# Kernel optimization log

Measured on AMD Instinct MI355X. Metric: run time of the kernel, lower is better.

The kernel has to match this reference:

```python
import jax, jax.numpy as jnp
import numpy as np

NEG_INF = -1e38


def wkv(k, v, w, u):
    """Log-sum-exp-stabilized RWKV WKV scan.
    k, v: (B, T, C); w, u: (C,). Returns y: (B, T, C).
    """
    B, T, C = k.shape

    def step(carry, kv_t):
        num, den, mx = carry            # each (B, C)
        k_t, v_t = kv_t                 # (B, C)
        ku = k_t + u
        m = jnp.maximum(mx, ku)
        e1 = jnp.exp(mx - m)
        e2 = jnp.exp(ku - m)
        y = (e1 * num + e2 * v_t) / (e1 * den + e2)
        # state update
        mw = mx + w
        m2 = jnp.maximum(mw, k_t)
        es1 = jnp.exp(mw - m2)
        es2 = jnp.exp(k_t - m2)
        num = es1 * num + es2 * v_t
        den = es1 * den + es2
        return (num, den, m2), y

    init = (jnp.zeros((B, C), k.dtype),
            jnp.zeros((B, C), k.dtype),
            jnp.full((B, C), NEG_INF, k.dtype))
    _, y = jax.lax.scan(step, init, (jnp.swapaxes(k, 0, 1), jnp.swapaxes(v, 0, 1)))
    return jnp.swapaxes(y, 0, 1)


def setup_inputs() -> dict:
    key = jax.random.key(0)
    ks = jax.random.split(key, 8)
    B, T, C = 8, 4096, 512
    x = jax.random.normal(ks[0], (B, T, C), dtype=jnp.float32)
    # Linear weights stored as (in, out) so forward is x @ W.
    W_rkv = jax.random.normal(ks[1], (C, 6 * C), dtype=jnp.float32) / np.sqrt(C)
    W_out = jax.random.normal(ks[2], (2 * C, C), dtype=jnp.float32) / np.sqrt(2 * C)
    time_decay = jax.random.uniform(ks[3], (C,), minval=-6.0, maxval=-5.0, dtype=jnp.float32)
    time_first = jax.random.uniform(ks[4], (C,), minval=-3.0, maxval=0.0, dtype=jnp.float32)
    time_decay_rev = jax.random.uniform(ks[5], (C,), minval=-6.0, maxval=-5.0, dtype=jnp.float32)
    time_first_rev = jax.random.uniform(ks[6], (C,), minval=-3.0, maxval=0.0, dtype=jnp.float32)
    return {"x": x, "W_rkv": W_rkv, "W_out": W_out,
            "time_decay": time_decay, "time_first": time_first,
            "time_decay_rev": time_decay_rev, "time_first_rev": time_first_rev}


def reference(x, W_rkv, W_out, time_decay, time_first, time_decay_rev, time_first_rev):
    B, T, C = x.shape
    rkv = (x @ W_rkv).reshape(B, T, 2, 3, C)
    # forward direction
    r_f, k_f, v_f = rkv[:, :, 0, 0], rkv[:, :, 0, 1], rkv[:, :, 0, 2]
    w_f = -jnp.exp(time_decay)
    out_f = jax.nn.sigmoid(r_f) * wkv(k_f, v_f, w_f, time_first)
    # backward direction (run scan on time-reversed k/v, then reverse back)
    r_b, k_b, v_b = rkv[:, :, 1, 0], rkv[:, :, 1, 1], rkv[:, :, 1, 2]
    w_b = -jnp.exp(time_decay_rev)
    out_b = wkv(k_b[:, ::-1], v_b[:, ::-1], w_b, time_first_rev)[:, ::-1]
    out_b = jax.nn.sigmoid(r_b) * out_b
    out_cat = jnp.concatenate([out_f, out_b], axis=-1)  # (B, T, 2C)
    return out_cat @ W_out
```

## Files before the change

kernel.cpp:

```cpp
#include <hip/hip_runtime.h>

typedef float f4 __attribute__((ext_vector_type(4)));
typedef unsigned short us4 __attribute__((ext_vector_type(4)));
typedef __bf16 bf16x8 __attribute__((ext_vector_type(8)));
typedef float f32x4 __attribute__((ext_vector_type(4)));
typedef _Float16 h8 __attribute__((ext_vector_type(8)));

#define TT 4096
#define CCH 512
#define NCH2 256
#define CHL2 16
#define NSEG 32
#define SEGC 8

__device__ __forceinline__ unsigned short f2bf(float f) {
  unsigned u = __builtin_bit_cast(unsigned, f);
  unsigned r = (u + 0x7FFFu + ((u >> 16) & 1u)) >> 16;
  return (unsigned short)r;
}
__device__ __forceinline__ void gload_lds16(const void* g, void* l) {
  __builtin_amdgcn_global_load_lds(
      (const __attribute__((address_space(1))) unsigned int*)g,
      (__attribute__((address_space(3))) unsigned int*)l, 16, 0, 0);
}
#define VMCNT(n) asm volatile("s_waitcnt vmcnt(" #n ")" ::: "memory")

__global__ __launch_bounds__(256)
void convert_f32_bf16(const float* __restrict__ in, unsigned short* __restrict__ out, int n4) {
  int i = blockIdx.x * 256 + threadIdx.x;
  if (i >= n4) return;
  f4 f = *(const f4*)(in + (size_t)i * 4);
  us4 o = { f2bf(f[0]), f2bf(f[1]), f2bf(f[2]), f2bf(f[3]) };
  *(us4*)(out + (size_t)i * 4) = o;
}

__global__ __launch_bounds__(256)
void transpose_to_bf16(const float* __restrict__ in, unsigned short* __restrict__ out,
                       int R, int Cc) {
  __shared__ unsigned short tile[32][33];
  int c0 = blockIdx.x * 32, r0 = blockIdx.y * 32;
  int tx = threadIdx.x, ty = threadIdx.y;
  #pragma unroll
  for (int j = 0; j < 32; j += 8)
    tile[ty + j][tx] = f2bf(in[(size_t)(r0 + ty + j) * Cc + c0 + tx]);
  __syncthreads();
  #pragma unroll
  for (int j = 0; j < 32; j += 8)
    out[(size_t)(c0 + ty + j) * R + r0 + tx] = tile[tx][ty + j];
}

__global__ __launch_bounds__(256)
void transpose_to_f16(const float* __restrict__ in, _Float16* __restrict__ out,
                      int R, int Cc) {
  __shared__ _Float16 tile[32][33];
  int c0 = blockIdx.x * 32, r0 = blockIdx.y * 32;
  int tx = threadIdx.x, ty = threadIdx.y;
  #pragma unroll
  for (int j = 0; j < 32; j += 8)
    tile[ty + j][tx] = (_Float16)in[(size_t)(r0 + ty + j) * Cc + c0 + tx];
  __syncthreads();
  #pragma unroll
  for (int j = 0; j < 32; j += 8)
    out[(size_t)(c0 + ty + j) * R + r0 + tx] = tile[tx][ty + j];
}

__global__ __launch_bounds__(512, 2)
void gemm256_g1(const unsigned short* __restrict__ A,
                const unsigned short* __restrict__ BT,
                _Float16* __restrict__ kbuf, _Float16* __restrict__ vbuf,
                _Float16* __restrict__ rbuf) {
  __shared__ char lds[131072];
  const int tid = threadIdx.x;
  const int lane = tid & 63, wv = tid >> 6;
  const int wm = wv >> 2, wn = wv & 3;
  const int ln15 = lane & 15, lq = lane >> 4;

  const int nwg = gridDim.x;
  const int bid = blockIdx.x;
  const int wgid = (nwg % 8 == 0) ? (bid % 8) * (nwg / 8) + bid / 8 : bid;
  const int bn = wgid % 12, bm = wgid / 12;
  const size_t m0 = (size_t)bm * 256, n0 = (size_t)bn * 256;
  const char* Ab = (const char*)(A + m0 * 512);
  const char* Bb = (const char*)(BT + n0 * 512);

  const int srow0 = tid >> 2, srow1 = 128 + (tid >> 2);
  const int sg = tid & 3;
  const int sgs0 = (sg ^ ((srow0 >> 1) & 3)) << 4;
  const int sgs1 = (sg ^ ((srow1 >> 1) & 3)) << 4;

  auto STAGE = [&](int mat, int t, int h) {
    const char* gsrc = mat ? Bb : Ab;
    char* ldst = lds + mat * 65536 + ((t & 1) << 15) + (h << 14);
    const size_t co = (size_t)t * 128 + (size_t)h * 64;
    gload_lds16(gsrc + (size_t)srow0 * 1024 + co + sgs0, ldst + tid * 16);
    gload_lds16(gsrc + (size_t)srow1 * 1024 + co + sgs1, ldst + 8192 + tid * 16);
  };

  f32x4 acc[8][4] = {};
  STAGE(0, 0, 0); STAGE(1, 0, 0); STAGE(0, 0, 1); STAGE(1, 0, 1);

  for (int t = 0; t < 8; ++t) {
    char* Abase = lds + ((t & 1) << 15);
    char* Bbase = lds + 65536 + ((t & 1) << 15);
    VMCNT(4);
    __builtin_amdgcn_s_barrier();
    __builtin_amdgcn_sched_barrier(0);
    {
      bf16x8 bf[4], af[8];
      #pragma unroll
      for (int fn = 0; fn < 4; ++fn) {
        const int r = wn * 64 + fn * 16 + ln15;
        bf[fn] = *(const bf16x8*)(Bbase + r * 64 + ((lq ^ ((r >> 1) & 3)) << 4));
      }
      #pragma unroll
      for (int fm = 0; fm < 8; ++fm) {
        const int r = wm * 128 + fm * 16 + ln15;
        af[fm] = *(const bf16x8*)(Abase + r * 64 + ((lq ^ ((r >> 1) & 3)) << 4));
      }
      if (t < 7) { STAGE(0, t + 1, 0); STAGE(1, t + 1, 0); }
      __builtin_amdgcn_s_setprio(1);
      #pragma unroll
      for (int fm = 0; fm < 8; ++fm)
        #pragma unroll
        for (int fn = 0; fn < 4; ++fn)
          acc[fm][fn] = __builtin_amdgcn_mfma_f32_16x16x32_bf16(af[fm], bf[fn], acc[fm][fn], 0, 0, 0);
      __builtin_amdgcn_s_setprio(0);
    }
    if (t < 7) { VMCNT(4); } else { VMCNT(0); }
    __builtin_amdgcn_s_barrier();
    __builtin_amdgcn_sched_barrier(0);
    {
      bf16x8 bf[4], af[8];
      #pragma unroll
      for (int fn = 0; fn < 4; ++fn) {
        const int r = wn * 64 + fn * 16 + ln15;
        bf[fn] = *(const bf16x8*)(Bbase + 16384 + r * 64 + ((lq ^ ((r >> 1) & 3)) << 4));
      }
      #pragma unroll
      for (int fm = 0; fm < 8; ++fm) {
        const int r = wm * 128 + fm * 16 + ln15;
        af[fm] = *(const bf16x8*)(Abase + 16384 + r * 64 + ((lq ^ ((r >> 1) & 3)) << 4));
      }
      if (t < 7) { STAGE(0, t + 1, 1); STAGE(1, t + 1, 1); }
      __builtin_amdgcn_s_setprio(1);
      #pragma unroll
      for (int fm = 0; fm < 8; ++fm)
        #pragma unroll
        for (int fn = 0; fn < 4; ++fn)
          acc[fm][fn] = __builtin_amdgcn_mfma_f32_16x16x32_bf16(af[fm], bf[fn], acc[fm][fn], 0, 0, 0);
      __builtin_amdgcn_s_setprio(0);
    }
  }

  const int n0i = (int)n0;
  const int dir = (n0i >= 1536) ? 1 : 0;
  const int jj0 = n0i - dir * 1536;
  const int seg = jj0 >> 9;
  const int cbase = jj0 & 511;
  _Float16* dbuf = (seg == 0) ? rbuf : (seg == 1 ? kbuf : vbuf);
  float* stg = (float*)lds;
  const int ebnd = wv >> 2;
  const int erow = (tid >> 3) & 31;
  const int el8 = tid & 7;
  __syncthreads();
  #pragma unroll
  for (int gi = 0; gi < 4; ++gi) {
    #pragma unroll
    for (int f2 = 0; f2 < 2; ++f2) {
      const int fm = gi * 2 + f2;
      #pragma unroll
      for (int q = 0; q < 4; ++q) {
        const int rloc = f2 * 16 + lq * 4 + q;
        float* dst = stg + wm * 8192 + rloc * 256;
        const int sw = ((rloc >> 2) & 1) << 4;
        #pragma unroll
        for (int fn = 0; fn < 4; ++fn)
          dst[(wn * 64 + fn * 16 + ln15) ^ sw] = acc[fm][fn][q];
      }
    }
    __syncthreads();
    {
      const int rowg = (int)m0 + ebnd * 128 + gi * 32 + erow;
      const int b_ = rowg >> 12, tt = rowg & 4095;
      const int trow = dir ? (4095 - tt) : tt;
      _Float16* gp = dbuf + ((size_t)(b_ * 2 + dir) * TT + trow) * 512 + cbase;
      const float* sp = stg + ebnd * 8192 + erow * 256;
      const int sw = ((erow >> 2) & 1) << 4;
      #pragma unroll
      for (int u = 0; u < 4; ++u) {
        const int cf = el8 * 8 + u * 64;
        const int cs = cf ^ sw;
        f4 a = *(const f4*)(sp + cs);
        f4 b = *(const f4*)(sp + cs + 4);
        h8 hv = { (_Float16)a[0], (_Float16)a[1], (_Float16)a[2], (_Float16)a[3],
                  (_Float16)b[0], (_Float16)b[1], (_Float16)b[2], (_Float16)b[3] };
        *(h8*)(gp + cf) = hv;
      }
    }
    __syncthreads();
  }
}

__global__ __launch_bounds__(512, 2)
void gemm2_256(const _Float16* __restrict__ obuf,
               const _Float16* __restrict__ BT,
               float* __restrict__ out) {
  __shared__ char lds[131072];
  const int tid = threadIdx.x;
  const int lane = tid & 63, wv = tid >> 6;
  const int wm = wv >> 2, wn = wv & 3;
  const int ln15 = lane & 15, lq = lane >> 4;

  const int nwg = gridDim.x;
  const int bid = blockIdx.x;
  const int wgid = (nwg % 8 == 0) ? (bid % 8) * (nwg / 8) + bid / 8 : bid;
  const int bn = wgid % 2, bm = wgid / 2;
  const size_t m0 = (size_t)bm * 256, n0 = (size_t)bn * 256;
  const int bB = (int)(m0 >> 12);
  const int tbase = (int)(m0 & 4095);
  const char* Bb = (const char*)(BT + n0 * 1024);

  const int srow0 = tid >> 2, srow1 = 128 + (tid >> 2);
  const int sg = tid & 3;
  const int sgs0 = (sg ^ ((srow0 >> 1) & 3)) << 4;
  const int sgs1 = (sg ^ ((srow1 >> 1) & 3)) << 4;

  auto STAGE = [&](int mat, int t, int h) {
    char* ldst = lds + mat * 65536 + ((t & 1) << 15) + (h << 14);
    if (mat == 0) {
      const int half = t >> 3;
      const char* Ah = (const char*)(obuf + (((size_t)(bB * 2 + half)) << 12) * 512);
      const size_t co = (size_t)(t & 7) * 128 + (size_t)h * 64;
      const size_t ar0 = half ? (size_t)(4095 - (tbase + srow0)) : (size_t)(tbase + srow0);
      const size_t ar1 = half ? (size_t)(4095 - (tbase + srow1)) : (size_t)(tbase + srow1);
      gload_lds16(Ah + ar0 * 1024 + co + sgs0, ldst + tid * 16);
      gload_lds16(Ah + ar1 * 1024 + co + sgs1, ldst + 8192 + tid * 16);
    } else {
      const size_t co = (size_t)t * 128 + (size_t)h * 64;
      gload_lds16(Bb + (size_t)srow0 * 2048 + co + sgs0, ldst + tid * 16);
      gload_lds16(Bb + (size_t)srow1 * 2048 + co + sgs1, ldst + 8192 + tid * 16);
    }
  };

  f32x4 acc[8][4] = {};
  STAGE(0, 0, 0); STAGE(1, 0, 0); STAGE(0, 0, 1); STAGE(1, 0, 1);

  for (int t = 0; t < 16; ++t) {
    char* Abase = lds + ((t & 1) << 15);
    char* Bbase = lds + 65536 + ((t & 1) << 15);
    VMCNT(4);
    __builtin_amdgcn_s_barrier();
    __builtin_amdgcn_sched_barrier(0);
    {
      h8 bf[4], af[8];
      #pragma unroll
      for (int fn = 0; fn < 4; ++fn) {
        const int r = wn * 64 + fn * 16 + ln15;
        bf[fn] = *(const h8*)(Bbase + r * 64 + ((lq ^ ((r >> 1) & 3)) << 4));
      }
      #pragma unroll
      for (int fm = 0; fm < 8; ++fm) {
        const int r = wm * 128 + fm * 16 + ln15;
        af[fm] = *(const h8*)(Abase + r * 64 + ((lq ^ ((r >> 1) & 3)) << 4));
      }
      if (t < 15) { STAGE(0, t + 1, 0); STAGE(1, t + 1, 0); }
      __builtin_amdgcn_s_setprio(1);
      #pragma unroll
      for (int fm = 0; fm < 8; ++fm)
        #pragma unroll
        for (int fn = 0; fn < 4; ++fn)
          acc[fm][fn] = __builtin_amdgcn_mfma_f32_16x16x32_f16(af[fm], bf[fn], acc[fm][fn], 0, 0, 0);
      __builtin_amdgcn_s_setprio(0);
    }
    if (t < 15) { VMCNT(4); } else { VMCNT(0); }
    __builtin_amdgcn_s_barrier();
    __builtin_amdgcn_sched_barrier(0);
    {
      h8 bf[4], af[8];
      #pragma unroll
      for (int fn = 0; fn < 4; ++fn) {
        const int r = wn * 64 + fn * 16 + ln15;
        bf[fn] = *(const h8*)(Bbase + 16384 + r * 64 + ((lq ^ ((r >> 1) & 3)) << 4));
      }
      #pragma unroll
      for (int fm = 0; fm < 8; ++fm) {
        const int r = wm * 128 + fm * 16 + ln15;
        af[fm] = *(const h8*)(Abase + 16384 + r * 64 + ((lq ^ ((r >> 1) & 3)) << 4));
      }
      if (t < 15) { STAGE(0, t + 1, 1); STAGE(1, t + 1, 1); }
      __builtin_amdgcn_s_setprio(1);
      #pragma unroll
      for (int fm = 0; fm < 8; ++fm)
        #pragma unroll
        for (int fn = 0; fn < 4; ++fn)
          acc[fm][fn] = __builtin_amdgcn_mfma_f32_16x16x32_f16(af[fm], bf[fn], acc[fm][fn], 0, 0, 0);
      __builtin_amdgcn_s_setprio(0);
    }
  }

  float* stg = (float*)lds;
  const int ebnd = wv >> 2;
  const int erow = (tid >> 3) & 31;
  const int el8 = tid & 7;
  __syncthreads();
  #pragma unroll
  for (int gi = 0; gi < 4; ++gi) {
    #pragma unroll
    for (int f2 = 0; f2 < 2; ++f2) {
      const int fm = gi * 2 + f2;
      #pragma unroll
      for (int q = 0; q < 4; ++q) {
        const int rloc = f2 * 16 + lq * 4 + q;
        float* dst = stg + wm * 8192 + rloc * 256;
        const int sw = ((rloc >> 2) & 1) << 4;
        #pragma unroll
        for (int fn = 0; fn < 4; ++fn)
          dst[(wn * 64 + fn * 16 + ln15) ^ sw] = acc[fm][fn][q];
      }
    }
    __syncthreads();
    {
      const int rowg = (int)m0 + ebnd * 128 + gi * 32 + erow;
      float* gp = out + (size_t)rowg * 512 + n0;
      const float* sp = stg + ebnd * 8192 + erow * 256;
      const int sw = ((erow >> 2) & 1) << 4;
      #pragma unroll
      for (int u = 0; u < 4; ++u) {
        const int cf = el8 * 8 + u * 64;
        const int cs = cf ^ sw;
        f4 a = *(const f4*)(sp + cs);
        f4 b = *(const f4*)(sp + cs + 4);
        *(f4*)(gp + cf) = a;
        *(f4*)(gp + cf + 4) = b;
      }
    }
    __syncthreads();
  }
}

__global__ __launch_bounds__(128)
void wkv_pass1(const _Float16* __restrict__ kbuf, const _Float16* __restrict__ vbuf,
               const float* __restrict__ td, const float* __restrict__ tdr,
               float* __restrict__ cN, float* __restrict__ cD, float* __restrict__ cM) {
  const int bd = blockIdx.x;
  const int ch = blockIdx.y * 2 + threadIdx.y;
  const int dir = bd & 1;
  const int c = threadIdx.x * 8;
  const float* tdp = (dir ? tdr : td) + c;
  float w[8], num[8], den[8], m[8];
  #pragma unroll
  for (int e = 0; e < 8; ++e) { w[e] = -__expf(tdp[e]); num[e] = 0.f; den[e] = 0.f; m[e] = -1e38f; }
  const size_t base = ((size_t)bd * TT + (size_t)ch * CHL2) * CCH + c;
  const _Float16* kp = kbuf + base;
  const _Float16* vp = vbuf + base;
  h8 ka = *(const h8*)(kp), va = *(const h8*)(vp);
  h8 kb = *(const h8*)(kp + CCH), vb = *(const h8*)(vp + CCH);
  for (int t = 0; t < CHL2; ++t) {
    h8 kc = {}, vc = {};
    if (t + 2 < CHL2) {
      kc = *(const h8*)(kp + (size_t)(t + 2) * CCH);
      vc = *(const h8*)(vp + (size_t)(t + 2) * CCH);
    }
    #pragma unroll
    for (int e = 0; e < 8; ++e) {
      float ke = (float)ka[e], ve = (float)va[e];
      float mw = m[e] + w[e];
      float m2 = fmaxf(mw, ke);
      float e1 = __expf(mw - m2), e2 = __expf(ke - m2);
      num[e] = e1 * num[e] + e2 * ve;
      den[e] = e1 * den[e] + e2;
      m[e] = m2;
    }
    ka = kb; va = vb; kb = kc; vb = vc;
  }
  const size_t ci = ((size_t)bd * NCH2 + ch) * CCH + c;
  #pragma unroll
  for (int h = 0; h < 2; ++h) {
    *(f4*)(cN + ci + h * 4) = (f4){num[h*4], num[h*4+1], num[h*4+2], num[h*4+3]};
    *(f4*)(cD + ci + h * 4) = (f4){den[h*4], den[h*4+1], den[h*4+2], den[h*4+3]};
    *(f4*)(cM + ci + h * 4) = (f4){m[h*4], m[h*4+1], m[h*4+2], m[h*4+3]};
  }
}

__global__ __launch_bounds__(128)
void wkv_p2a(const float* __restrict__ td, const float* __restrict__ tdr,
             const float* __restrict__ cN, const float* __restrict__ cD,
             const float* __restrict__ cM,
             float* __restrict__ scN, float* __restrict__ scD, float* __restrict__ scM) {
  const int bd = blockIdx.x, seg = blockIdx.y;
  const int dir = bd & 1;
  const int c = threadIdx.x * 4;
  f4 tdv = *(const f4*)((dir ? tdr : td) + c);
  float dw[4], num[4], den[4], m[4];
  #pragma unroll
  for (int e = 0; e < 4; ++e) { dw[e] = -__expf(tdv[e]) * (float)CHL2; num[e] = 0.f; den[e] = 0.f; m[e] = -1e38f; }
  size_t ci = ((size_t)bd * NCH2 + (size_t)seg * SEGC) * CCH + c;
  for (int j = 0; j < SEGC; ++j, ci += CCH) {
    f4 ln = *(const f4*)(cN + ci);
    f4 ld = *(const f4*)(cD + ci);
    f4 lm = *(const f4*)(cM + ci);
    #pragma unroll
    for (int e = 0; e < 4; ++e) {
      float mp = m[e] + dw[e];
      float mm = fmaxf(mp, lm[e]);
      float e1 = __expf(mp - mm), e2 = __expf(lm[e] - mm);
      num[e] = e1 * num[e] + e2 * ln[e];
      den[e] = e1 * den[e] + e2 * ld[e];
      m[e] = mm;
    }
  }
  const size_t si = ((size_t)bd * NSEG + seg) * CCH + c;
  *(f4*)(scN + si) = (f4){num[0], num[1], num[2], num[3]};
  *(f4*)(scD + si) = (f4){den[0], den[1], den[2], den[3]};
  *(f4*)(scM + si) = (f4){m[0], m[1], m[2], m[3]};
}

__global__ __launch_bounds__(128)
void wkv_p2b(const float* __restrict__ td, const float* __restrict__ tdr,
             float* __restrict__ scN, float* __restrict__ scD, float* __restrict__ scM) {
  const int bd = blockIdx.x;
  const int dir = bd & 1;
  const int c = threadIdx.x * 4;
  f4 tdv = *(const f4*)((dir ? tdr : td) + c);
  float dws[4], num[4], den[4], m[4];
  #pragma unroll
  for (int e = 0; e < 4; ++e) { dws[e] = -__expf(tdv[e]) * (float)(CHL2 * SEGC); num[e] = 0.f; den[e] = 0.f; m[e] = -1e38f; }
  size_t si = (size_t)bd * NSEG * CCH + c;
  for (int s = 0; s < NSEG; ++s, si += CCH) {
    f4 ln = *(const f4*)(scN + si);
    f4 ld = *(const f4*)(scD + si);
    f4 lm = *(const f4*)(scM + si);
    *(f4*)(scN + si) = (f4){num[0], num[1], num[2], num[3]};
    *(f4*)(scD + si) = (f4){den[0], den[1], den[2], den[3]};
    *(f4*)(scM + si) = (f4){m[0], m[1], m[2], m[3]};
    #pragma unroll
    for (int e = 0; e < 4; ++e) {
      float mp = m[e] + dws[e];
      float mm = fmaxf(mp, lm[e]);
      float e1 = __expf(mp - mm), e2 = __expf(lm[e] - mm);
      num[e] = e1 * num[e] + e2 * ln[e];
      den[e] = e1 * den[e] + e2 * ld[e];
      m[e] = mm;
    }
  }
}

__global__ __launch_bounds__(128)
void wkv_p2c(const float* __restrict__ td, const float* __restrict__ tdr,
             const float* __restrict__ scN, const float* __restrict__ scD,
             const float* __restrict__ scM,
             float* __restrict__ cN, float* __restrict__ cD, float* __restrict__ cM) {
  const int bd = blockIdx.x, seg = blockIdx.y;
  const int dir = bd & 1;
  const int c = threadIdx.x * 4;
  f4 tdv = *(const f4*)((dir ? tdr : td) + c);
  const size_t si = ((size_t)bd * NSEG + seg) * CCH + c;
  f4 nv = *(const f4*)(scN + si);
  f4 dv = *(const f4*)(scD + si);
  f4 mv = *(const f4*)(scM + si);
  float dw[4], num[4], den[4], m[4];
  #pragma unroll
  for (int e = 0; e < 4; ++e) {
    dw[e] = -__expf(tdv[e]) * (float)CHL2;
    num[e] = nv[e]; den[e] = dv[e]; m[e] = mv[e];
  }
  size_t ci = ((size_t)bd * NCH2 + (size_t)seg * SEGC) * CCH + c;
  for (int j = 0; j < SEGC; ++j, ci += CCH) {
    f4 ln = *(const f4*)(cN + ci);
    f4 ld = *(const f4*)(cD + ci);
    f4 lm = *(const f4*)(cM + ci);
    *(f4*)(cN + ci) = (f4){num[0], num[1], num[2], num[3]};
    *(f4*)(cD + ci) = (f4){den[0], den[1], den[2], den[3]};
    *(f4*)(cM + ci) = (f4){m[0], m[1], m[2], m[3]};
    #pragma unroll
    for (int e = 0; e < 4; ++e) {
      float mp = m[e] + dw[e];
      float mm = fmaxf(mp, lm[e]);
      float e1 = __expf(mp - mm), e2 = __expf(lm[e] - mm);
      num[e] = e1 * num[e] + e2 * ln[e];
      den[e] = e1 * den[e] + e2 * ld[e];
      m[e] = mm;
    }
  }
}

__global__ __launch_bounds__(128)
void wkv_pass3(const _Float16* __restrict__ kbuf, const _Float16* __restrict__ vbuf,
               _Float16* __restrict__ rbuf,
               const float* __restrict__ td, const float* __restrict__ tf,
               const float* __restrict__ tdr, const float* __restrict__ tfr,
               const float* __restrict__ cN, const float* __restrict__ cD,
               const float* __restrict__ cM) {
  const int bd = blockIdx.x;
  const int ch = blockIdx.y * 2 + threadIdx.y;
  const int dir = bd & 1;
  const int c = threadIdx.x * 8;
  const float* tdp = (dir ? tdr : td) + c;
  const float* tup = (dir ? tfr : tf) + c;
  const size_t ci = ((size_t)bd * NCH2 + ch) * CCH + c;
  float w[8], u[8], num[8], den[8], m[8];
  #pragma unroll
  for (int e = 0; e < 8; ++e) {
    w[e] = -__expf(tdp[e]); u[e] = tup[e];
    num[e] = cN[ci + e]; den[e] = cD[ci + e]; m[e] = cM[ci + e];
  }
  const size_t base = ((size_t)bd * TT + (size_t)ch * CHL2) * CCH + c;
  const _Float16* kp = kbuf + base;
  const _Float16* vp = vbuf + base;
  _Float16* rp = rbuf + base;
  h8 ka = *(const h8*)(kp), va = *(const h8*)(vp), ra = *(const h8*)(rp);
  h8 kb = *(const h8*)(kp + CCH), vb = *(const h8*)(vp + CCH), rb = *(const h8*)(rp + CCH);
  for (int t = 0; t < CHL2; ++t) {
    h8 kc = {}, vc = {}, rc = {};
    if (t + 2 < CHL2) {
      kc = *(const h8*)(kp + (size_t)(t + 2) * CCH);
      vc = *(const h8*)(vp + (size_t)(t + 2) * CCH);
      rc = *(const h8*)(rp + (size_t)(t + 2) * CCH);
    }
    _Float16 o[8];
    #pragma unroll
    for (int e = 0; e < 8; ++e) {
      float ke = (float)ka[e], ve = (float)va[e];
      float ku = ke + u[e];
      float mm = fmaxf(m[e], ku);
      float e1 = __expf(m[e] - mm), e2 = __expf(ku - mm);
      float y = (e1 * num[e] + e2 * ve) * __builtin_amdgcn_rcpf(e1 * den[e] + e2);
      float rt = (float)ra[e];
      float sig = __builtin_amdgcn_rcpf(1.f + __expf(-rt));
      o[e] = (_Float16)(sig * y);
      float mw = m[e] + w[e];
      float m2 = fmaxf(mw, ke);
      float es1 = __expf(mw - m2), es2 = __expf(ke - m2);
      num[e] = es1 * num[e] + es2 * ve;
      den[e] = es1 * den[e] + es2;
      m[e] = m2;
    }
    h8 ov = { o[0], o[1], o[2], o[3], o[4], o[5], o[6], o[7] };
    *(h8*)(rp + (size_t)t * CCH) = ov;
    ka = kb; va = vb; ra = rb; kb = kc; vb = vc; rb = rc;
  }
}

extern "C" void kernel_launch(void* const* d_in, const int* in_sizes, int n_in,
                              void* d_out, int out_size, void* d_ws, size_t ws_size,
                              hipStream_t stream) {
  const float* x   = (const float*)d_in[0];
  const float* Wr  = (const float*)d_in[1];
  const float* Wo  = (const float*)d_in[2];
  const float* td  = (const float*)d_in[3];
  const float* tf  = (const float*)d_in[4];
  const float* tdr = (const float*)d_in[5];
  const float* tfr = (const float*)d_in[6];
  float* out = (float*)d_out;

  auto rnd = [](size_t b) { return (b + 255) & ~(size_t)255; };
  const size_t wBytes = rnd((size_t)3072 * 512 * 2) + rnd((size_t)512 * 1024 * 2);
  auto need = [&](int Bs) {
    size_t s = wBytes;
    s += 3 * rnd((size_t)Bs * 2 * TT * 512 * 2);
    s += rnd((size_t)Bs * TT * 512 * 2);
    return s;
  };
  int Bs = 8;
  while (Bs > 1 && need(Bs) > ws_size) Bs >>= 1;

  char* ws = (char*)d_ws;
  size_t off = 0;
  auto alloc = [&](size_t bytes) -> char* {
    char* p = ws + off;
    off += (bytes + 255) & ~(size_t)255;
    return p;
  };
  unsigned short* wrkvT = (unsigned short*)alloc((size_t)3072 * 512 * 2);
  _Float16*       woutT = (_Float16*)alloc((size_t)512 * 1024 * 2);
  _Float16*       kbuf  = (_Float16*)alloc((size_t)Bs * 2 * TT * 512 * 2);
  _Float16*       vbuf  = (_Float16*)alloc((size_t)Bs * 2 * TT * 512 * 2);
  _Float16*       rbuf  = (_Float16*)alloc((size_t)Bs * 2 * TT * 512 * 2);
  unsigned short* xb    = (unsigned short*)alloc((size_t)Bs * TT * 512 * 2);
  const size_t cs = (size_t)Bs * 2 * NCH2 * 512;
  const size_t ss = (size_t)Bs * 2 * NSEG * 512;
  float* cN  = (float*)xb;
  float* cD  = cN + cs;
  float* cM  = cD + cs;
  float* scN = cM + cs;
  float* scD = scN + ss;
  float* scM = scD + ss;

  transpose_to_bf16<<<dim3(3072 / 32, 512 / 32), dim3(32, 8), 0, stream>>>(Wr, wrkvT, 512, 3072);
  transpose_to_f16<<<dim3(512 / 32, 1024 / 32), dim3(32, 8), 0, stream>>>(Wo, woutT, 1024, 512);

  const int nslices = 8 / Bs;
  const int Mslice = Bs * TT;
  const int mt256 = Mslice >> 8;
  for (int s = 0; s < nslices; ++s) {
    const float* xs = x + (size_t)s * Mslice * 512;
    float* outs = out + (size_t)s * Mslice * 512;
    convert_f32_bf16<<<Mslice * 512 / 1024, 256, 0, stream>>>(xs, xb, Mslice * 512 / 4);
    gemm256_g1<<<mt256 * 12, 512, 0, stream>>>(xb, wrkvT, kbuf, vbuf, rbuf);
    wkv_pass1<<<dim3(Bs * 2, NCH2 / 2), dim3(64, 2), 0, stream>>>(kbuf, vbuf, td, tdr, cN, cD, cM);
    wkv_p2a<<<dim3(Bs * 2, NSEG), 128, 0, stream>>>(td, tdr, cN, cD, cM, scN, scD, scM);
    wkv_p2b<<<Bs * 2, 128, 0, stream>>>(td, tdr, scN, scD, scM);
    wkv_p2c<<<dim3(Bs * 2, NSEG), 128, 0, stream>>>(td, tdr, scN, scD, scM, cN, cD, cM);
    wkv_pass3<<<dim3(Bs * 2, NCH2 / 2), dim3(64, 2), 0, stream>>>(kbuf, vbuf, rbuf, td, tf, tdr, tfr,
                                                                  cN, cD, cM);
    gemm2_256<<<mt256 * 2, 512, 0, stream>>>(rbuf, woutT, outs);
  }
}
```

Before: 301.1 us.

## Fuse three-kernel chunk-state prefix scan into one per-channel kernel

Replaces the three-stage prefix (segment reduce, segment scan, segment apply) with a single kernel. Each thread handles one channel and keeps the segment carries in shared memory. This removes two kernel launches and the global-memory round trip for the segment states. In exchange, each thread does a much longer serial dependent chain, with scalar loads and far fewer blocks, which reduces parallelism.

```diff
diff --git a/kernel.cpp b/kernel.cpp
--- a/kernel.cpp
+++ b/kernel.cpp
@@ -383,103 +383,46 @@
 }
 
 __global__ __launch_bounds__(128)
-void wkv_p2a(const float* __restrict__ td, const float* __restrict__ tdr,
-             const float* __restrict__ cN, const float* __restrict__ cD,
-             const float* __restrict__ cM,
-             float* __restrict__ scN, float* __restrict__ scD, float* __restrict__ scM) {
-  const int bd = blockIdx.x, seg = blockIdx.y;
+void wkv_pass2f(const float* __restrict__ td, const float* __restrict__ tdr,
+                float* __restrict__ cN, float* __restrict__ cD, float* __restrict__ cM) {
+  __shared__ float sN[NSEG][128], sD[NSEG][128], sM[NSEG][128];
+  const int bd = blockIdx.x, cg = blockIdx.y;
   const int dir = bd & 1;
-  const int c = threadIdx.x * 4;
-  f4 tdv = *(const f4*)((dir ? tdr : td) + c);
-  float dw[4], num[4], den[4], m[4];
-  #pragma unroll
-  for (int e = 0; e < 4; ++e) { dw[e] = -__expf(tdv[e]) * (float)CHL2; num[e] = 0.f; den[e] = 0.f; m[e] = -1e38f; }
-  size_t ci = ((size_t)bd * NCH2 + (size_t)seg * SEGC) * CCH + c;
-  for (int j = 0; j < SEGC; ++j, ci += CCH) {
-    f4 ln = *(const f4*)(cN + ci);
-    f4 ld = *(const f4*)(cD + ci);
-    f4 lm = *(const f4*)(cM + ci);
-    #pragma unroll
-    for (int e = 0; e < 4; ++e) {
-      float mp = m[e] + dw[e];
-      float mm = fmaxf(mp, lm[e]);
-      float e1 = __expf(mp - mm), e2 = __expf(lm[e] - mm);
-      num[e] = e1 * num[e] + e2 * ln[e];
-      den[e] = e1 * den[e] + e2 * ld[e];
-      m[e] = mm;
-    }
-  }
-  const size_t si = ((size_t)bd * NSEG + seg) * CCH + c;
-  *(f4*)(scN + si) = (f4){num[0], num[1], num[2], num[3]};
-  *(f4*)(scD + si) = (f4){den[0], den[1], den[2], den[3]};
-  *(f4*)(scM + si) = (f4){m[0], m[1], m[2], m[3]};
-}
-
-__global__ __launch_bounds__(128)
-void wkv_p2b(const float* __restrict__ td, const float* __restrict__ tdr,
-             float* __restrict__ scN, float* __restrict__ scD, float* __restrict__ scM) {
-  const int bd = blockIdx.x;
-  const int dir = bd & 1;
-  const int c = threadIdx.x * 4;
-  f4 tdv = *(const f4*)((dir ? tdr : td) + c);
-  float dws[4], num[4], den[4], m[4];
-  #pragma unroll
-  for (int e = 0; e < 4; ++e) { dws[e] = -__expf(tdv[e]) * (float)(CHL2 * SEGC); num[e] = 0.f; den[e] = 0.f; m[e] = -1e38f; }
-  size_t si = (size_t)bd * NSEG * CCH + c;
-  for (int s = 0; s < NSEG; ++s, si += CCH) {
-    f4 ln = *(const f4*)(scN + si);
-    f4 ld = *(const f4*)(scD + si);
-    f4 lm = *(const f4*)(scM + si);
-    *(f4*)(scN + si) = (f4){num[0], num[1], num[2], num[3]};
-    *(f4*)(scD + si) = (f4){den[0], den[1], den[2], den[3]};
-    *(f4*)(scM + si) = (f4){m[0], m[1], m[2], m[3]};
-    #pragma unroll
-    for (int e = 0; e < 4; ++e) {
-      float mp = m[e] + dws[e];
-      float mm = fmaxf(mp, lm[e]);
-      float e1 = __expf(mp - mm), e2 = __expf(lm[e] - mm);
-      num[e] = e1 * num[e] + e2 * ln[e];
-      den[e] = e1 * den[e] + e2 * ld[e];
-      m[e] = mm;
-    }
-  }
-}
-
-__global__ __launch_bounds__(128)
-void wkv_p2c(const float* __restrict__ td, const float* __restrict__ tdr,
-             const float* __restrict__ scN, const float* __restrict__ scD,
-             const float* __restrict__ scM,
-             float* __restrict__ cN, float* __restrict__ cD, float* __restrict__ cM) {
-  const int bd = blockIdx.x, seg = blockIdx.y;
-  const int dir = bd & 1;
-  const int c = threadIdx.x * 4;
-  f4 tdv = *(const f4*)((dir ? tdr : td) + c);
-  const size_t si = ((size_t)bd * NSEG + seg) * CCH + c;
-  f4 nv = *(const f4*)(scN + si);
-  f4 dv = *(const f4*)(scD + si);
-  f4 mv = *(const f4*)(scM + si);
-  float dw[4], num[4], den[4], m[4];
-  #pragma unroll
-  for (int e = 0; e < 4; ++e) {
-    dw[e] = -__expf(tdv[e]) * (float)CHL2;
-    num[e] = nv[e]; den[e] = dv[e]; m[e] = mv[e];
-  }
-  size_t ci = ((size_t)bd * NCH2 + (size_t)seg * SEGC) * CCH + c;
-  for (int j = 0; j < SEGC; ++j, ci += CCH) {
-    f4 ln = *(const f4*)(cN + ci);
-    f4 ld = *(const f4*)(cD + ci);
-    f4 lm = *(const f4*)(cM + ci);
-    *(f4*)(cN + ci) = (f4){num[0], num[1], num[2], num[3]};
-    *(f4*)(cD + ci) = (f4){den[0], den[1], den[2], den[3]};
-    *(f4*)(cM + ci) = (f4){m[0], m[1], m[2], m[3]};
-    #pragma unroll
-    for (int e = 0; e < 4; ++e) {
-      float mp = m[e] + dw[e];
-      float mm = fmaxf(mp, lm[e]);
-      float e1 = __expf(mp - mm), e2 = __expf(lm[e] - mm);
-      num[e] = e1 * num[e] + e2 * ln[e];
-      den[e] = e1 * den[e] + e2 * ld[e];
-      m[e] = mm;
+  const int tx = threadIdx.x;
+  const int c = cg * 128 + tx;
+  const float wchl = -__expf((dir ? tdr : td)[c]) * (float)CHL2;
+  const float wseg = wchl * (float)SEGC;
+  const size_t base = (size_t)bd * NCH2 * CCH + c;
+  for (int seg = 0; seg < NSEG; ++seg) {
+    float n = 0.f, d = 0.f, m = -1e38f;
+    size_t ci = base + (size_t)seg * SEGC * CCH;
+    for (int j = 0; j < SEGC; ++j, ci += CCH) {
+      float ln = cN[ci], ld = cD[ci], lm = cM[ci];
+      float mp = m + wchl, mm = fmaxf(mp, lm);
+      float e1 = __expf(mp - mm), e2 = __expf(lm - mm);
+      n = e1 * n + e2 * ln; d = e1 * d + e2 * ld; m = mm;
+    }
+    sN[seg][tx] = n; sD[seg][tx] = d; sM[seg][tx] = m;
+  }
+  {
+    float n = 0.f, d = 0.f, m = -1e38f;
+    for (int seg = 0; seg < NSEG; ++seg) {
+      float tn = sN[seg][tx], tdv = sD[seg][tx], tm = sM[seg][tx];
+      sN[seg][tx] = n; sD[seg][tx] = d; sM[seg][tx] = m;
+      float mp = m + wseg, mm = fmaxf(mp, tm);
+      float e1 = __expf(mp - mm), e2 = __expf(tm - mm);
+      n = e1 * n + e2 * tn; d = e1 * d + e2 * tdv; m = mm;
+    }
+  }
+  for (int seg = 0; seg < NSEG; ++seg) {
+    float n = sN[seg][tx], d = sD[seg][tx], m = sM[seg][tx];
+    size_t ci = base + (size_t)seg * SEGC * CCH;
+    for (int j = 0; j < SEGC; ++j, ci += CCH) {
+      float ln = cN[ci], ld = cD[ci], lm = cM[ci];
+      cN[ci] = n; cD[ci] = d; cM[ci] = m;
+      float mp = m + wchl, mm = fmaxf(mp, lm);
+      float e1 = __expf(mp - mm), e2 = __expf(lm - mm);
+      n = e1 * n + e2 * ln; d = e1 * d + e2 * ld; m = mm;
     }
   }
 }
@@ -578,13 +521,9 @@
   _Float16*       rbuf  = (_Float16*)alloc((size_t)Bs * 2 * TT * 512 * 2);
   unsigned short* xb    = (unsigned short*)alloc((size_t)Bs * TT * 512 * 2);
   const size_t cs = (size_t)Bs * 2 * NCH2 * 512;
-  const size_t ss = (size_t)Bs * 2 * NSEG * 512;
   float* cN  = (float*)xb;
   float* cD  = cN + cs;
   float* cM  = cD + cs;
-  float* scN = cM + cs;
-  float* scD = scN + ss;
-  float* scM = scD + ss;
 
   transpose_to_bf16<<<dim3(3072 / 32, 512 / 32), dim3(32, 8), 0, stream>>>(Wr, wrkvT, 512, 3072);
   transpose_to_f16<<<dim3(512 / 32, 1024 / 32), dim3(32, 8), 0, stream>>>(Wo, woutT, 1024, 512);
@@ -598,9 +537,7 @@
     convert_f32_bf16<<<Mslice * 512 / 1024, 256, 0, stream>>>(xs, xb, Mslice * 512 / 4);
     gemm256_g1<<<mt256 * 12, 512, 0, stream>>>(xb, wrkvT, kbuf, vbuf, rbuf);
     wkv_pass1<<<dim3(Bs * 2, NCH2 / 2), dim3(64, 2), 0, stream>>>(kbuf, vbuf, td, tdr, cN, cD, cM);
-    wkv_p2a<<<dim3(Bs * 2, NSEG), 128, 0, stream>>>(td, tdr, cN, cD, cM, scN, scD, scM);
-    wkv_p2b<<<Bs * 2, 128, 0, stream>>>(td, tdr, scN, scD, scM);
-    wkv_p2c<<<dim3(Bs * 2, NSEG), 128, 0, stream>>>(td, tdr, scN, scD, scM, cN, cD, cM);
+    wkv_pass2f<<<dim3(Bs * 2, 4), 128, 0, stream>>>(td, tdr, cN, cD, cM);
     wkv_pass3<<<dim3(Bs * 2, NCH2 / 2), dim3(64, 2), 0, stream>>>(kbuf, vbuf, rbuf, td, tf, tdr, tfr,
                                                                   cN, cD, cM);
     gemm2_256<<<mt256 * 2, 512, 0, stream>>>(rbuf, woutT, outs);
```

Result: slower. 317.9 us (+5.6%).
